# Kernel tuning notes

Hardware: AMD Instinct MI355X
Metric: run time of the kernel (lower is better)

## Reference

```python
import jax, jax.numpy as jnp
import numpy as np

B, C, FS, Z_DIM, OUT_C, F_SIZE = 256, 512, 16, 64, 1, 3
NZ = FS * FS  # 256


def setup_inputs() -> dict:
    key = jax.random.key(0)
    k1, k2, k3, k4, k5 = jax.random.split(key, 5)
    # z: [B, C, H, W]
    z = jax.random.normal(k1, (B, C, FS, FS), dtype=jnp.float32)
    # 512 independent per-channel Linear(Nz -> z_dim): stacked weights/biases
    lim_in = 1.0 / np.sqrt(NZ)
    W_in = jax.random.uniform(k2, (C, NZ, Z_DIM), minval=-lim_in, maxval=lim_in, dtype=jnp.float32)
    b_in = jax.random.uniform(k3, (C, Z_DIM), minval=-lim_in, maxval=lim_in, dtype=jnp.float32)
    # shared Linear(z_dim -> out_channels*f_size*f_size)
    lim_out = 1.0 / np.sqrt(Z_DIM)
    W_out = jax.random.uniform(k4, (Z_DIM, OUT_C * F_SIZE * F_SIZE), minval=-lim_out, maxval=lim_out, dtype=jnp.float32)
    b_out = jax.random.uniform(k5, (OUT_C * F_SIZE * F_SIZE,), minval=-lim_out, maxval=lim_out, dtype=jnp.float32)
    return {"z": z, "W_in": W_in, "b_in": b_in, "W_out": W_out, "b_out": b_out}


def reference(z, W_in, b_in, W_out, b_out):
    batch = z.shape[0]
    # flatten each channel's HxW map: [B, C, Nz]
    x = z.reshape(batch, C, NZ)
    # per-channel Linear as one batched GEMM: [B, C, z_dim]
    a = jnp.einsum('bcn,cnz->bcz', x, W_in) + b_in[None, :, :]
    # shared output Linear: [B, C, out_c*f*f]
    k = jnp.einsum('bcz,zk->bck', a, W_out) + b_out
    # [B, C, out_channels, f_size, f_size]
    return k.reshape(batch, C, OUT_C, F_SIZE, F_SIZE)
```

## Files before the change

kernel.cpp:

```cpp
#include <hip/hip_runtime.h>

#define BB 256
#define CC 512
#define NZ 256
#define ZD 64
#define KK 9

template<int CTRL>
__device__ __forceinline__ float dpp_add(float v) {
    int o = __builtin_amdgcn_update_dpp(0, __float_as_int(v), CTRL, 0xF, 0xF, true);
    return v + __int_as_float(o);
}
__device__ __forceinline__ float red8(float v) {
    v = dpp_add<0xB1>(v);
    v = dpp_add<0x4E>(v);
    v = dpp_add<0x141>(v);
    return v;
}

typedef __attribute__((address_space(1))) const void gconst_t;
typedef __attribute__((address_space(3))) void lds_t;
__device__ __forceinline__ void load_row_to_lds(const float* gp, float* lp) {
    __builtin_amdgcn_global_load_lds((gconst_t*)gp, (lds_t*)lp, 16, 0, 0);
}

__global__ __launch_bounds__(512, 2)
void wf_kernel(const float* __restrict__ W_in,
               const float* __restrict__ b_in,
               const float* __restrict__ W_out,
               const float* __restrict__ b_out,
               float* __restrict__ wf,
               float* __restrict__ bk) {
    __shared__ __align__(16) float s_woutT[KK * ZD];
    __shared__ float s_bin[ZD];

    const int c = blockIdx.x;
    const int t = threadIdx.x;

    for (int i = t; i < KK * ZD; i += 512) {
        float v = W_out[i];
        int zz = i / KK, k = i - zz * KK;
        s_woutT[k * ZD + zz] = v;
    }
    if (t < ZD) s_bin[t] = b_in[c * ZD + t];
    __syncthreads();

    const int n = t >> 1, half = t & 1;
    const float* wrow = W_in + ((size_t)c * NZ + n) * ZD + half * 32;
    float acc[KK];
#pragma unroll
    for (int k = 0; k < KK; ++k) acc[k] = 0.f;
#pragma unroll
    for (int j = 0; j < 8; ++j) {
        const float4 w = *reinterpret_cast<const float4*>(wrow + 4 * j);
#pragma unroll
        for (int k = 0; k < KK; ++k) {
            const float4 wo = *reinterpret_cast<const float4*>(
                &s_woutT[k * ZD + half * 32 + 4 * j]);
            acc[k] += w.x * wo.x + w.y * wo.y + w.z * wo.z + w.w * wo.w;
        }
    }
#pragma unroll
    for (int k = 0; k < KK; ++k) acc[k] = dpp_add<0xB1>(acc[k]);
    if (half == 0) {
#pragma unroll
        for (int k = 0; k < KK; ++k) wf[((size_t)c * KK + k) * NZ + n] = acc[k];
    }
    if (t < KK) {
        float s = 0.f;
        for (int zz = 0; zz < ZD; ++zz) s += s_bin[zz] * s_woutT[t * ZD + zz];
        bk[c * KK + t] = s + b_out[t];
    }
}

__global__ __launch_bounds__(256, 2)
void out_kernel(const float* __restrict__ z,
                const float* __restrict__ wf,
                const float* __restrict__ bk,
                float* __restrict__ out) {
    __shared__ __align__(16) float s_wfT[KK * NZ];
    __shared__ float s_biask[KK];
    __shared__ __align__(16) float s_z[2][32 * NZ];

    const int c = blockIdx.x;
    const int bh = blockIdx.y;
    const int t = threadIdx.x;
    const int lane = t & 63;
    const int wave = t >> 6;
    const int g = lane >> 3;
    const int sub = lane & 7;

    const size_t bstr = (size_t)CC * NZ;
    const float* zc = z + (size_t)c * NZ;
    const int base_b = bh * 128;

    {
        const float4* src = reinterpret_cast<const float4*>(wf + (size_t)c * KK * NZ);
        float4* dst = reinterpret_cast<float4*>(s_wfT);
        for (int i = t; i < KK * NZ / 4; i += 256) dst[i] = src[i];
        if (t < KK) s_biask[t] = bk[c * KK + t];
    }
    __syncthreads();

    const float biasS = s_biask[sub];
    const float bias8 = s_biask[8];

#pragma unroll
    for (int i = 0; i < 8; ++i) {
        const int r = wave * 8 + i;
        load_row_to_lds(zc + (size_t)(base_b + r) * bstr + lane * 4,
                        &s_z[0][r * NZ]);
    }
#pragma unroll
    for (int i = 0; i < 8; ++i) {
        const int r = wave * 8 + i;
        load_row_to_lds(zc + (size_t)(base_b + 32 + r) * bstr + lane * 4,
                        &s_z[1][r * NZ]);
    }

    float vsel[4], v8[4];

#pragma unroll
    for (int s = 0; s < 4; ++s) {
        const int cur = s & 1;

        if (s < 3) {
            asm volatile("s_waitcnt vmcnt(8)" ::: "memory");
        } else {
            asm volatile("s_waitcnt vmcnt(0)" ::: "memory");
        }
        __builtin_amdgcn_sched_barrier(0);

        const float* xrow = &s_z[cur][(wave * 8 + g) * NZ];
        float acc[KK];
#pragma unroll
        for (int k = 0; k < KK; ++k) acc[k] = 0.f;
#pragma unroll
        for (int j = 0; j < 8; ++j) {
            const float4 x = *reinterpret_cast<const float4*>(
                &xrow[j * 32 + sub * 4]);
#pragma unroll
            for (int k = 0; k < KK; ++k) {
                const float4 w = *reinterpret_cast<const float4*>(
                    &s_wfT[k * NZ + j * 32 + sub * 4]);
                acc[k] += x.x * w.x + x.y * w.y + x.z * w.z + x.w * w.w;
            }
        }
#pragma unroll
        for (int k = 0; k < KK; ++k) acc[k] = red8(acc[k]);

        float v = acc[0];
#pragma unroll
        for (int k = 1; k < 8; ++k) {
            if (sub == k) v = acc[k];
        }
        vsel[s] = v;
        v8[s] = acc[8];

        if (s < 2) {
            asm volatile("s_waitcnt lgkmcnt(0)" ::: "memory");
            __builtin_amdgcn_sched_barrier(0);
#pragma unroll
            for (int i = 0; i < 8; ++i) {
                const int r = wave * 8 + i;
                load_row_to_lds(
                    zc + (size_t)(base_b + (s + 2) * 32 + r) * bstr + lane * 4,
                    &s_z[cur][r * NZ]);
            }
        }
    }

#pragma unroll
    for (int s = 0; s < 4; ++s) {
        const int b = base_b + s * 32 + wave * 8 + g;
        const size_t o0 = ((size_t)b * CC + c) * KK;
        out[o0 + sub] = vsel[s] + biasS;
        if (sub == 0) out[o0 + 8] = v8[s] + bias8;
    }
}

__global__ __launch_bounds__(512, 2)
void hyper_kernel(const float* __restrict__ z,
                  const float* __restrict__ W_in,
                  const float* __restrict__ b_in,
                  const float* __restrict__ W_out,
                  const float* __restrict__ b_out,
                  float* __restrict__ out) {
    __shared__ __align__(16) float s_wfT[KK * NZ];
    __shared__ __align__(16) float s_woutT[KK * ZD];
    __shared__ float s_bin[ZD];
    __shared__ float s_biask[KK];

    const int c = blockIdx.x;
    const int t = threadIdx.x;

    for (int i = t; i < KK * ZD; i += 512) {
        float v = W_out[i];
        int zz = i / KK, k = i - zz * KK;
        s_woutT[k * ZD + zz] = v;
    }
    if (t < ZD) s_bin[t] = b_in[c * ZD + t];
    __syncthreads();

    {
        const int n = t >> 1, half = t & 1;
        const float* wrow = W_in + ((size_t)c * NZ + n) * ZD + half * 32;
        float acc[KK];
#pragma unroll
        for (int k = 0; k < KK; ++k) acc[k] = 0.f;
#pragma unroll
        for (int j = 0; j < 8; ++j) {
            const float4 w = *reinterpret_cast<const float4*>(wrow + 4 * j);
#pragma unroll
            for (int k = 0; k < KK; ++k) {
                const float4 wo = *reinterpret_cast<const float4*>(
                    &s_woutT[k * ZD + half * 32 + 4 * j]);
                acc[k] += w.x * wo.x + w.y * wo.y + w.z * wo.z + w.w * wo.w;
            }
        }
#pragma unroll
        for (int k = 0; k < KK; ++k) acc[k] = dpp_add<0xB1>(acc[k]);
        if (half == 0) {
#pragma unroll
            for (int k = 0; k < KK; ++k) s_wfT[k * NZ + n] = acc[k];
        }
        if (t < KK) {
            float s = 0.f;
            for (int zz = 0; zz < ZD; ++zz) s += s_bin[zz] * s_woutT[t * ZD + zz];
            s_biask[t] = s + b_out[t];
        }
    }
    __syncthreads();

    const int lane = t & 63;
    const int wave = t >> 6;
    const int g = lane >> 3;
    const int sub = lane & 7;
    const int b0 = wave * 32 + g * 4;
    const float biasS = s_biask[sub];
    const float bias8 = s_biask[8];

    const float* xp = z + ((size_t)b0 * CC + c) * NZ + sub * 4;
    const size_t bstr = (size_t)CC * NZ;

    float acc[4][KK];
#pragma unroll
    for (int bb = 0; bb < 4; ++bb)
#pragma unroll
        for (int k = 0; k < KK; ++k) acc[bb][k] = 0.f;

    float4 xb[2][4];
#pragma unroll
    for (int bb = 0; bb < 4; ++bb)
        xb[0][bb] = *reinterpret_cast<const float4*>(xp + bb * bstr);

#pragma unroll
    for (int j = 0; j < 8; ++j) {
        if (j < 7) {
#pragma unroll
            for (int bb = 0; bb < 4; ++bb)
                xb[(j + 1) & 1][bb] =
                    *reinterpret_cast<const float4*>(xp + bb * bstr + (j + 1) * 32);
        }
#pragma unroll
        for (int k = 0; k < KK; ++k) {
            const float4 wfv = *reinterpret_cast<const float4*>(
                &s_wfT[k * NZ + sub * 4 + j * 32]);
#pragma unroll
            for (int bb = 0; bb < 4; ++bb) {
                const float4 x = xb[j & 1][bb];
                acc[bb][k] += x.x * wfv.x + x.y * wfv.y + x.z * wfv.z + x.w * wfv.w;
            }
        }
    }

#pragma unroll
    for (int bb = 0; bb < 4; ++bb)
#pragma unroll
        for (int k = 0; k < KK; ++k) acc[bb][k] = red8(acc[bb][k]);

#pragma unroll
    for (int bb = 0; bb < 4; ++bb) {
        float v = acc[bb][0];
#pragma unroll
        for (int k = 1; k < 8; ++k) {
            if (sub == k) v = acc[bb][k];
        }
        const size_t o0 = ((size_t)(b0 + bb) * CC + c) * KK;
        out[o0 + sub] = v + biasS;
        if (sub == 0) out[o0 + 8] = acc[bb][8] + bias8;
    }
}

extern "C" void kernel_launch(void* const* d_in, const int* in_sizes, int n_in,
                              void* d_out, int out_size, void* d_ws, size_t ws_size,
                              hipStream_t stream) {
    const float* z     = (const float*)d_in[0];
    const float* W_in  = (const float*)d_in[1];
    const float* b_in  = (const float*)d_in[2];
    const float* W_out = (const float*)d_in[3];
    const float* b_out = (const float*)d_in[4];
    float* out = (float*)d_out;

    const size_t WF_ELTS = (size_t)CC * KK * NZ;
    const size_t BK_ELTS = (size_t)CC * KK;
    const size_t NEED = (WF_ELTS + BK_ELTS) * sizeof(float);

    if (d_ws != nullptr && ws_size >= NEED) {
        float* wfp = (float*)d_ws;
        float* bkp = wfp + WF_ELTS;
        wf_kernel<<<dim3(CC), dim3(512), 0, stream>>>(W_in, b_in, W_out, b_out, wfp, bkp);
        out_kernel<<<dim3(CC, 2), dim3(256), 0, stream>>>(z, wfp, bkp, out);
    } else {
        hyper_kernel<<<dim3(CC), dim3(512), 0, stream>>>(z, W_in, b_in, W_out, b_out, out);
    }
}
```

Measured before the change: 236.6 us.

## Tile out_kernel over 8-channel groups with contiguous z slabs and interleaved wf layout

Reorganizes the folded weight buffer so each block of 8 channels has its weights interleaved by chunk, and changes out_kernel to process 8 consecutive channels per block. Each wave loads a contiguous 8KB z slab (8 channels of one batch) instead of strided single-channel rows, which is meant to improve DRAM access locality and coalescing of output writes. Launch bounds drop to occupancy 1 because LDS use grows (wf tile 72KB plus z buffers), and the grid changes to 64x16 blocks.

```diff
diff --git a/kernel.cpp b/kernel.cpp
--- a/kernel.cpp
+++ b/kernel.cpp
@@ -5,6 +5,9 @@
 #define NZ 256
 #define ZD 64
 #define KK 9
+#define CT 8
+#define NCT (CC / CT)
+#define WFT (KK * CT * 32)
 
 template<int CTRL>
 __device__ __forceinline__ float dpp_add(float v) {
@@ -20,7 +23,7 @@
 
 typedef __attribute__((address_space(1))) const void gconst_t;
 typedef __attribute__((address_space(3))) void lds_t;
-__device__ __forceinline__ void load_row_to_lds(const float* gp, float* lp) {
+__device__ __forceinline__ void load_1k_to_lds(const float* gp, float* lp) {
     __builtin_amdgcn_global_load_lds((gconst_t*)gp, (lds_t*)lp, 16, 0, 0);
 }
 
@@ -36,6 +39,7 @@
 
     const int c = blockIdx.x;
     const int t = threadIdx.x;
+    const int ct = c >> 3, cc = c & 7;
 
     for (int i = t; i < KK * ZD; i += 512) {
         float v = W_out[i];
@@ -63,8 +67,10 @@
 #pragma unroll
     for (int k = 0; k < KK; ++k) acc[k] = dpp_add<0xB1>(acc[k]);
     if (half == 0) {
-#pragma unroll
-        for (int k = 0; k < KK; ++k) wf[((size_t)c * KK + k) * NZ + n] = acc[k];
+        const int j = n >> 5, nn = n & 31;
+#pragma unroll
+        for (int k = 0; k < KK; ++k)
+            wf[(((size_t)ct * KK + k) * 8 + j) * 256 + cc * 32 + nn] = acc[k];
     }
     if (t < KK) {
         float s = 0.f;
@@ -73,76 +79,71 @@
     }
 }
 
-__global__ __launch_bounds__(256, 2)
+__global__ __launch_bounds__(256, 1)
 void out_kernel(const float* __restrict__ z,
                 const float* __restrict__ wf,
                 const float* __restrict__ bk,
                 float* __restrict__ out) {
-    __shared__ __align__(16) float s_wfT[KK * NZ];
-    __shared__ float s_biask[KK];
-    __shared__ __align__(16) float s_z[2][32 * NZ];
-
-    const int c = blockIdx.x;
-    const int bh = blockIdx.y;
+    __shared__ __align__(16) float s_wf[KK * 8 * 256];
+    __shared__ float s_biask[CT][KK];
+    __shared__ __align__(16) float s_z[4][2][8 * 256];
+
+    const int ct = blockIdx.x;
+    const int bt = blockIdx.y;
+    const int c0 = ct * CT;
     const int t = threadIdx.x;
     const int lane = t & 63;
     const int wave = t >> 6;
     const int g = lane >> 3;
     const int sub = lane & 7;
 
-    const size_t bstr = (size_t)CC * NZ;
-    const float* zc = z + (size_t)c * NZ;
-    const int base_b = bh * 128;
-
     {
-        const float4* src = reinterpret_cast<const float4*>(wf + (size_t)c * KK * NZ);
-        float4* dst = reinterpret_cast<float4*>(s_wfT);
-        for (int i = t; i < KK * NZ / 4; i += 256) dst[i] = src[i];
-        if (t < KK) s_biask[t] = bk[c * KK + t];
-    }
+        const float* src = wf + (size_t)ct * (KK * 8 * 256);
+        for (int q = wave * 18; q < wave * 18 + 18; ++q)
+            load_1k_to_lds(src + q * 256 + lane * 4, &s_wf[q * 256]);
+    }
+    if (t < CT * KK) s_biask[t / KK][t % KK] = bk[(c0 + t / KK) * KK + t % KK];
     __syncthreads();
 
-    const float biasS = s_biask[sub];
-    const float bias8 = s_biask[8];
-
-#pragma unroll
-    for (int i = 0; i < 8; ++i) {
-        const int r = wave * 8 + i;
-        load_row_to_lds(zc + (size_t)(base_b + r) * bstr + lane * 4,
-                        &s_z[0][r * NZ]);
-    }
-#pragma unroll
-    for (int i = 0; i < 8; ++i) {
-        const int r = wave * 8 + i;
-        load_row_to_lds(zc + (size_t)(base_b + 32 + r) * bstr + lane * 4,
-                        &s_z[1][r * NZ]);
-    }
+    const float biasS = s_biask[g][sub];
+    const float bias8 = s_biask[g][8];
+
+    const int bq = bt * 16 + wave;
+    const float* zb0 = z + ((size_t)bq * CC + c0) * NZ;
+    const size_t sstr = (size_t)4 * CC * NZ;
+    const size_t lsw = (size_t)(lane >> 3) * NZ + (lane & 7) * 4;
+
+    float* const slab0 = s_z[wave][0];
+    float* const slab1 = s_z[wave][1];
+
+#pragma unroll
+    for (int q = 0; q < 8; ++q)
+        load_1k_to_lds(zb0 + lsw + q * 32, &slab0[q * 256]);
+#pragma unroll
+    for (int q = 0; q < 8; ++q)
+        load_1k_to_lds(zb0 + sstr + lsw + q * 32, &slab1[q * 256]);
 
     float vsel[4], v8[4];
 
 #pragma unroll
     for (int s = 0; s < 4; ++s) {
-        const int cur = s & 1;
-
-        if (s < 3) {
-            asm volatile("s_waitcnt vmcnt(8)" ::: "memory");
-        } else {
-            asm volatile("s_waitcnt vmcnt(0)" ::: "memory");
-        }
+        float* const slab = (s & 1) ? slab1 : slab0;
+
+        if (s < 3) asm volatile("s_waitcnt vmcnt(8)" ::: "memory");
+        else       asm volatile("s_waitcnt vmcnt(0)" ::: "memory");
         __builtin_amdgcn_sched_barrier(0);
 
-        const float* xrow = &s_z[cur][(wave * 8 + g) * NZ];
         float acc[KK];
 #pragma unroll
         for (int k = 0; k < KK; ++k) acc[k] = 0.f;
 #pragma unroll
         for (int j = 0; j < 8; ++j) {
             const float4 x = *reinterpret_cast<const float4*>(
-                &xrow[j * 32 + sub * 4]);
+                &slab[j * 256 + lane * 4]);
 #pragma unroll
             for (int k = 0; k < KK; ++k) {
                 const float4 w = *reinterpret_cast<const float4*>(
-                    &s_wfT[k * NZ + j * 32 + sub * 4]);
+                    &s_wf[(k * 8 + j) * 256 + lane * 4]);
                 acc[k] += x.x * w.x + x.y * w.y + x.z * w.z + x.w * w.w;
             }
         }
@@ -160,20 +161,17 @@
         if (s < 2) {
             asm volatile("s_waitcnt lgkmcnt(0)" ::: "memory");
             __builtin_amdgcn_sched_barrier(0);
-#pragma unroll
-            for (int i = 0; i < 8; ++i) {
-                const int r = wave * 8 + i;
-                load_row_to_lds(
-                    zc + (size_t)(base_b + (s + 2) * 32 + r) * bstr + lane * 4,
-                    &s_z[cur][r * NZ]);
-            }
+            const float* zn = zb0 + (size_t)(s + 2) * sstr;
+#pragma unroll
+            for (int q = 0; q < 8; ++q)
+                load_1k_to_lds(zn + lsw + q * 32, &slab[q * 256]);
         }
     }
 
 #pragma unroll
     for (int s = 0; s < 4; ++s) {
-        const int b = base_b + s * 32 + wave * 8 + g;
-        const size_t o0 = ((size_t)b * CC + c) * KK;
+        const int b = bq + s * 4;
+        const size_t o0 = ((size_t)b * CC + c0 + g) * KK;
         out[o0 + sub] = vsel[s] + biasS;
         if (sub == 0) out[o0 + 8] = v8[s] + bias8;
     }
@@ -302,7 +300,7 @@
     const float* b_out = (const float*)d_in[4];
     float* out = (float*)d_out;
 
-    const size_t WF_ELTS = (size_t)CC * KK * NZ;
+    const size_t WF_ELTS = (size_t)NCT * KK * 8 * 256;
     const size_t BK_ELTS = (size_t)CC * KK;
     const size_t NEED = (WF_ELTS + BK_ELTS) * sizeof(float);
 
@@ -310,7 +308,7 @@
         float* wfp = (float*)d_ws;
         float* bkp = wfp + WF_ELTS;
         wf_kernel<<<dim3(CC), dim3(512), 0, stream>>>(W_in, b_in, W_out, b_out, wfp, bkp);
-        out_kernel<<<dim3(CC, 2), dim3(256), 0, stream>>>(z, wfp, bkp, out);
+        out_kernel<<<dim3(NCT, BB / 16), dim3(256), 0, stream>>>(z, wfp, bkp, out);
     } else {
         hyper_kernel<<<dim3(CC), dim3(512), 0, stream>>>(z, W_in, b_in, W_out, b_out, out);
     }
```

After: 238.1 us. Within noise of the previous version (+0.6%).
